# Optimization experiments

Measured on AMD Instinct MI355X. Metric: run time of the kernel, lower is better.

The kernel has to match this reference:

```python
import jax, jax.numpy as jnp
import numpy as np
import math


def _conv(x, w, scale, bias, stride=1):
    # Ultralytics-style Conv: Conv2d(bias=False, pad=k//2) + BatchNorm (folded into
    # per-channel scale/bias) + SiLU
    k = w.shape[-1]
    p = k // 2
    y = jax.lax.conv_general_dilated(x, w, (stride, stride), [(p, p), (p, p)],
                                     dimension_numbers=('NCHW', 'OIHW', 'NCHW'))
    y = y * scale[None, :, None, None] + bias[None, :, None, None]
    return y * jax.nn.sigmoid(y)


def setup_inputs() -> dict:
    key = jax.random.key(0)
    ks = jax.random.split(key, 24)
    B, CH1, CH2, H1, W1, HW = 32, 512, 512, 20, 20, 40
    EMB = 256
    s = 0.05
    half = CH1 // 2
    d = {}
    d['x1'] = jax.random.normal(ks[0], (B, CH1, H1, W1), jnp.float32)
    d['x2'] = jax.random.normal(ks[1], (B, CH2, HW, HW), jnp.float32)
    # CrossAttention params
    d['q_w'] = jax.random.normal(ks[2], (EMB, CH1, 3, 3)) * s
    d['q_s'] = 1.0 + jax.random.normal(ks[3], (EMB,)) * s
    d['q_b'] = jax.random.normal(ks[4], (EMB,)) * s
    d['key_w'] = jax.random.normal(ks[5], (EMB, CH2)) * s
    # MGFAB / CSHA params (CA = channel-MLP sigmoid gate, rate=4)
    d['ca_w1'] = jax.random.normal(ks[6], (half // 4, half)) * s
    d['ca_b1'] = jnp.zeros((half // 4,))
    d['ca_w2'] = jax.random.normal(ks[7], (half, half // 4)) * s
    d['ca_b2'] = jnp.zeros((half,))
    d['sa1_w'] = jax.random.normal(ks[8], (half, half, 3, 3)) * s
    d['sa1_s'] = 1.0 + jax.random.normal(ks[9], (half,)) * s
    d['sa1_b'] = jax.random.normal(ks[10], (half,)) * s
    d['sa2_w'] = jax.random.normal(ks[11], (half, half, 3, 3)) * s
    d['sa2_s'] = 1.0 + jax.random.normal(ks[12], (half,)) * s
    d['sa2_b'] = jax.random.normal(ks[13], (half,)) * s
    d['conv2_w'] = jax.random.normal(ks[14], (CH1, 3 * half, 1, 1)) * s
    d['conv2_s'] = 1.0 + jax.random.normal(ks[15], (CH1,)) * s
    d['conv2_b'] = jax.random.normal(ks[16], (CH1,)) * s
    # conv3 branch (single Conv since patch_size[0] < 5)
    d['c3_w'] = jax.random.normal(ks[17], (CH2, CH2, 3, 3)) * s
    d['c3_s'] = 1.0 + jax.random.normal(ks[18], (CH2,)) * s
    d['c3_b'] = jax.random.normal(ks[19], (CH2,)) * s
    return d


def _forward(x1, x2, q_w, q_s, q_b, key_w, ca_w1, ca_b1, ca_w2, ca_b2,
             sa1_w, sa1_s, sa1_b, sa2_w, sa2_s, sa2_b,
             conv2_w, conv2_s, conv2_b, c3_w, c3_s, c3_b):
    NH, PH, PW = 8, 4, 4
    b, c, h, w = x2.shape
    cH = c // NH                       # channels per head
    nph, npw = h // PH, w // PW        # patch grid
    L = nph * npw                      # number of patches == number of q tokens

    # ---- CrossAttention ----
    # value: per-head flattened patches [b*NH, L, cH*PH*PW] (row-major over h,w)
    v = x2.reshape(b * NH, cH, nph, PH, npw, PW).transpose(0, 2, 4, 1, 3, 5)
    v = v.reshape(b * NH, L, cH * PH * PW)
    # key: avg-pool each patch -> linear(c -> emb) -> split heads
    kp = x2.reshape(b, c, nph, PH, npw, PW).mean(axis=(3, 5))  # [b, c, nph, npw]
    k = jnp.einsum('bcl,ec->ble', kp.reshape(b, c, L), key_w)  # [b, L, EMB]
    dh = k.shape[-1] // NH
    k = k.reshape(b, L, NH, dh).transpose(0, 2, 1, 3).reshape(b * NH, L, dh)
    # query: stride-2 conv on x1 -> tokens -> split heads
    q = _conv(x1, q_w, q_s, q_b, stride=2)                     # [b, EMB, nph, npw]
    q = q.reshape(b, -1, L).transpose(0, 2, 1)                 # [b, L, EMB]
    q = q.reshape(b, L, NH, dh).transpose(0, 2, 1, 3).reshape(b * NH, L, dh)
    score = jnp.einsum('nqd,nkd->nqk', q, k) / math.sqrt(dh)
    wts = jax.nn.softmax(score, axis=-1)                       # dropout = identity (eval)
    y = jnp.einsum('nqk,nkv->nqv', wts, v)                     # [b*NH, L, cH*PH*PW]
    # reassemble patches back into [b, c, h, w]
    attn = y.reshape(b, NH, nph, npw, cH, PH, PW).transpose(0, 1, 4, 2, 5, 3, 6)
    attn = attn.reshape(b, c, h, w)

    # ---- conv3 branch with residual ----
    x2_out = _conv(attn, c3_w, c3_s, c3_b) + attn

    x1_up = jnp.repeat(jnp.repeat(x1, 2, axis=2), 2, axis=3)   # [b, ch1, h, w]
    half = x1_up.shape[1] // 2
    a0, a1 = x1_up[:, :half], x1_up[:, half:]
    # CA: channel MLP gate
    xp = a1.transpose(0, 2, 3, 1)                              # [b, h, w, half]
    att = jnp.maximum(xp @ ca_w1.T + ca_b1, 0.0) @ ca_w2.T + ca_b2
    x_ca = a1 * jax.nn.sigmoid(att.transpose(0, 3, 1, 2))
    # SA: two 3x3 Convs + residual
    x_sa = _conv(_conv(x_ca, sa1_w, sa1_s, sa1_b), sa2_w, sa2_s, sa2_b)
    a2 = x_sa + x_ca
    cat = jnp.concatenate([a0, a1, a2], axis=1)                # [b, 3*half, h, w]
    x1_out = _conv(cat, conv2_w, conv2_s, conv2_b)             # [b, ch1, h, w]

    return jnp.concatenate([x1_out, x2_out], axis=1)           # [b, ch1+ch2, h, w]


def reference(x1, x2, q_w, q_s, q_b, key_w, ca_w1, ca_b1, ca_w2, ca_b2,
              sa1_w, sa1_s, sa1_b, sa2_w, sa2_s, sa2_b,
              conv2_w, conv2_s, conv2_b, c3_w, c3_s, c3_b):
    return _forward(x1, x2, q_w, q_s, q_b, key_w, ca_w1, ca_b1, ca_w2, ca_b2,
                    sa1_w, sa1_s, sa1_b, sa2_w, sa2_s, sa2_b,
                    conv2_w, conv2_s, conv2_b, c3_w, c3_s, c3_b)
```

## Files before the change

kernel.cpp:

```cpp
#include <hip/hip_runtime.h>
#include <hip/hip_bf16.h>

using bf16 = __hip_bfloat16;
using bf16x2 = __hip_bfloat162;
typedef __attribute__((ext_vector_type(8))) short short8;
typedef __attribute__((ext_vector_type(4))) float f32x4;

__device__ __forceinline__ float b2f(bf16 v) { return __bfloat162float(v); }
__device__ __forceinline__ bf16 f2b(float v) { return __float2bfloat16(v); }

__device__ __forceinline__ void gload_lds16(const bf16* g, bf16* l)
{
    __builtin_amdgcn_global_load_lds(
        (const __attribute__((address_space(1))) void*)g,
        (__attribute__((address_space(3))) void*)l,
        16, 0, 0);
}

#define PH_BAR() do { __builtin_amdgcn_sched_barrier(0); __builtin_amdgcn_s_barrier(); __builtin_amdgcn_sched_barrier(0); } while (0)
#define WAIT_LGKM0() do { asm volatile("s_waitcnt lgkmcnt(0)" ::: "memory"); __builtin_amdgcn_sched_barrier(0); } while (0)
#define WAIT_VM0() do { asm volatile("s_waitcnt vmcnt(0)" ::: "memory"); __builtin_amdgcn_sched_barrier(0); } while (0)
#define WAIT_VM2() do { asm volatile("s_waitcnt vmcnt(2)" ::: "memory"); __builtin_amdgcn_sched_barrier(0); } while (0)
#define WAIT_VM4() do { asm volatile("s_waitcnt vmcnt(4)" ::: "memory"); __builtin_amdgcn_sched_barrier(0); } while (0)

__global__ __launch_bounds__(256) void nchw_to_nhwc(const float* __restrict__ in,
                                                    bf16* __restrict__ out,
                                                    int C, int H, int W, int pad)
{
    __shared__ bf16 tile[64][68];
    const int S = H * W;
    const int HP = H + 2 * pad, WP = W + 2 * pad;
    const int b = blockIdx.x, s0 = blockIdx.y * 64, c0 = blockIdx.z * 64;
    const int t = threadIdx.x;
    const int a = t & 63, q = t >> 6;
#pragma unroll
    for (int i = 0; i < 16; ++i) {
        int cl = q + i * 4;
        int s = s0 + a;
        tile[cl][a] = (s < S) ? f2b(in[((size_t)b * C + c0 + cl) * S + s]) : f2b(0.f);
    }
    __syncthreads();
#pragma unroll
    for (int i = 0; i < 16; ++i) {
        int sl = q + i * 4;
        int s = s0 + sl;
        if (s < S) {
            int y = s / W, x = s - (s / W) * W;
            out[(((size_t)b * HP + y + pad) * WP + x + pad) * C + c0 + a] = tile[a][sl];
        }
    }
}

__global__ __launch_bounds__(256) void halo_zero(bf16* __restrict__ buf, int W, int C)
{
    const int b = blockIdx.x, y = blockIdx.y;
    const int P = W + 2;
    const bf16 z = f2b(0.f);
    bf16* row = buf + ((size_t)b * P + y) * P * C;
    if (y == 0 || y == P - 1) {
        for (int i = threadIdx.x; i < P * C; i += 256) row[i] = z;
    } else {
        for (int i = threadIdx.x; i < 2 * C; i += 256) {
            const int x = (i < C) ? 0 : P - 1;
            const int c = (i < C) ? i : i - C;
            row[(size_t)x * C + c] = z;
        }
    }
}

__global__ __launch_bounds__(256) void pack_out(const bf16* __restrict__ x1o,
                                                const bf16* __restrict__ x2o,
                                                float* __restrict__ out)
{
    __shared__ bf16 tile[64][68];
    const int b = blockIdx.x, s0 = blockIdx.y * 64, ch0 = blockIdx.z * 64;
    const bf16* src = (ch0 < 512) ? x1o : x2o;
    const int c0 = ch0 & 511;
    const int t = threadIdx.x;
    const int a = t & 63, q = t >> 6;
#pragma unroll
    for (int i = 0; i < 16; ++i) {
        int sl = q + i * 4;
        tile[sl][a] = src[((size_t)b * 1600 + s0 + sl) * 512 + c0 + a];
    }
    __syncthreads();
#pragma unroll
    for (int i = 0; i < 16; ++i) {
        int cl = q + i * 4;
        out[((size_t)b * 1024 + ch0 + cl) * 1600 + s0 + a] = b2f(tile[a][cl]);
    }
}

__global__ __launch_bounds__(256) void reorder_w(const float* __restrict__ w,
                                                 bf16* __restrict__ wr,
                                                 int C, int total)
{
    int i = blockIdx.x * 256 + threadIdx.x;
    if (i >= total) return;
    int nineC = 9 * C;
    int o = i / nineC;
    int r = i - o * nineC;
    int tap = r / C;
    int c = r - tap * C;
    wr[i] = f2b(w[((size_t)o * C + c) * 9 + tap]);
}

__global__ __launch_bounds__(256) void f32_to_bf16(const float* __restrict__ in,
                                                   bf16* __restrict__ out, int n)
{
    int i = blockIdx.x * 256 + threadIdx.x;
    if (i < n) out[i] = f2b(in[i]);
}

__global__ __launch_bounds__(256) void pool_kp(const bf16* __restrict__ x2n,
                                               bf16* __restrict__ kp)
{
    const int p = blockIdx.x;
    const int b = p / 100, l = p - (p / 100) * 100;
    const int ph = l / 10, pw = l - (l / 10) * 10;
    const int t = threadIdx.x;
    const bf16x2* base = (const bf16x2*)(x2n + (((size_t)(b * 40 + ph * 4) * 40) + pw * 4) * 512) + t;
    float sx = 0.f, sy = 0.f;
#pragma unroll
    for (int py = 0; py < 4; ++py)
#pragma unroll
        for (int px = 0; px < 4; ++px) {
            float2 v = __bfloat1622float2(base[(py * 40 + px) * 256]);
            sx += v.x; sy += v.y;
        }
    ((bf16x2*)(kp + (size_t)p * 512))[t] = __float22bfloat162_rn(make_float2(sx * 0.0625f, sy * 0.0625f));
}

__global__ __launch_bounds__(256) void ca_mlp(const bf16* __restrict__ x1n,
                                              const float* __restrict__ w1, const float* __restrict__ b1,
                                              const float* __restrict__ w2, const float* __restrict__ b2,
                                              bf16* __restrict__ xca)
{
    __shared__ float a1v[256];
    __shared__ float part[4][64];
    __shared__ float hid[64];
    const int blk = blockIdx.x;
    const int b = blk / 400;
    const int rem = blk - b * 400;
    const int y = rem / 20, x = rem - (rem / 20) * 20;
    const int t = threadIdx.x;
    const bf16* src = x1n + ((size_t)(b * 22 + y + 1) * 22 + x + 1) * 512 + 256;
    a1v[t] = b2f(src[t]);
    __syncthreads();
    {
        const int h = t & 63, seg = t >> 6;
        float acc = 0.f;
        const float* wp = w1 + (size_t)h * 256 + seg * 64;
        const float* ap = a1v + seg * 64;
#pragma unroll 8
        for (int c = 0; c < 64; ++c) acc += wp[c] * ap[c];
        part[seg][h] = acc;
    }
    __syncthreads();
    if (t < 64)
        hid[t] = fmaxf(part[0][t] + part[1][t] + part[2][t] + part[3][t] + b1[t], 0.f);
    __syncthreads();
    float acc2 = b2[t];
    const float* w2p = w2 + (size_t)t * 64;
#pragma unroll 8
    for (int h = 0; h < 64; ++h) acc2 += w2p[h] * hid[h];
    const float g = 1.f / (1.f + __expf(-acc2));
    const bf16 o = f2b(a1v[t] * g);
    const size_t obase = ((size_t)(b * 42 + 2 * y + 1) * 42 + 2 * x + 1) * 256 + t;
    xca[obase] = o;
    xca[obase + 256] = o;
    xca[obase + 42 * 256] = o;
    xca[obase + 42 * 256 + 256] = o;
}

__global__ __launch_bounds__(256, 1)
void attn_kernel(const float* __restrict__ q, const float* __restrict__ k,
                 const bf16* __restrict__ x2n, bf16* __restrict__ attn)
{
    __shared__ float sc[100][100];
    __shared__ bf16 wT[100][104];
    const int t = threadIdx.x;
    const int n = blockIdx.x;
    const int b = n >> 3, hd = n & 7;
    const float* qn = q + (size_t)n * 3200;
    const float* kn = k + (size_t)n * 3200;
    for (int e = t; e < 10000; e += 256) {
        const int i = e / 100;
        const int j = e - i * 100;
        const float4* qa = (const float4*)(qn + i * 32);
        const float4* ka = (const float4*)(kn + j * 32);
        float d = 0.f;
#pragma unroll
        for (int u = 0; u < 8; ++u) {
            float4 xv = qa[u], yv = ka[u];
            d += xv.x * yv.x + xv.y * yv.y + xv.z * yv.z + xv.w * yv.w;
        }
        sc[i][j] = d * 0.17677669529663687f;
    }
    __syncthreads();
    if (t < 100) {
        float mx = -1e30f;
        for (int j = 0; j < 100; ++j) mx = fmaxf(mx, sc[t][j]);
        float s = 0.f;
        for (int j = 0; j < 100; ++j) s += __expf(sc[t][j] - mx);
        const float inv = 1.f / s;
        for (int j = 0; j < 100; ++j) wT[j][t] = f2b(__expf(sc[t][j] - mx) * inv);
    }
    __syncthreads();
    const int ch0 = (t & 15) * 4;
    const int pix = t >> 4;
    const int py = pix >> 2, px = pix & 3;
    const bf16* vbase = x2n + (((size_t)(b * 40 + py) * 40) + px) * 512 + hd * 64 + ch0;
    for (int ql0 = 0; ql0 < 100; ql0 += 20) {
        float2 a0[20], a1[20];
#pragma unroll
        for (int i = 0; i < 20; ++i) { a0[i] = make_float2(0.f, 0.f); a1[i] = make_float2(0.f, 0.f); }
        for (int l = 0; l < 100; ++l) {
            const int ph = l / 10, pw = l - (l / 10) * 10;
            const bf16* vp = vbase + ((size_t)(ph * 160 + pw * 4)) * 512;
            const float2 v01 = __bfloat1622float2(*(const bf16x2*)vp);
            const float2 v23 = __bfloat1622float2(*(const bf16x2*)(vp + 2));
            const bf16x2* wp = (const bf16x2*)&wT[l][ql0];
#pragma unroll
            for (int ii = 0; ii < 10; ++ii) {
                const float2 w2 = __bfloat1622float2(wp[ii]);
                a0[ii * 2 + 0].x += w2.x * v01.x; a0[ii * 2 + 0].y += w2.x * v01.y;
                a1[ii * 2 + 0].x += w2.x * v23.x; a1[ii * 2 + 0].y += w2.x * v23.y;
                a0[ii * 2 + 1].x += w2.y * v01.x; a0[ii * 2 + 1].y += w2.y * v01.y;
                a1[ii * 2 + 1].x += w2.y * v23.x; a1[ii * 2 + 1].y += w2.y * v23.y;
            }
        }
#pragma unroll
        for (int i = 0; i < 20; ++i) {
            const int ql = ql0 + i;
            const int ph = ql / 10, pw = ql - (ql / 10) * 10;
            bf16* op = attn + (((size_t)(b * 42 + ph * 4 + py + 1) * 42) + pw * 4 + px + 1) * 512 + hd * 64 + ch0;
            *(bf16x2*)op = __float22bfloat162_rn(a0[i]);
            *(bf16x2*)(op + 2) = __float22bfloat162_rn(a1[i]);
        }
    }
}

enum ConvMode { M_QCONV = 0, M_SA1 = 1, M_SA2 = 2, M_C3 = 3, M_CONV2 = 4, M_KPROJ = 5 };

template <int MODE>
__global__ __launch_bounds__(256, 2)
void conv_mfma(const bf16* __restrict__ in, const bf16* __restrict__ wr,
               const float* __restrict__ scale, const float* __restrict__ bias,
               float* __restrict__ outf)
{
    constexpr int CIN  = 512;
    constexpr int TAPS = (MODE == M_KPROJ) ? 1 : 9;
    constexpr int STR  = 2;
    constexpr int HP   = 22;
    constexpr int WOUT = 10;
    constexpr int K    = TAPS * CIN;
    constexpr int KD   = (TAPS == 9) ? 3 : 1;

    __shared__ bf16 Al[128][64];
    __shared__ bf16 Bl[128][64];

    const int t = threadIdx.x;
    const int p0 = blockIdx.x * 128;
    const int n0 = blockIdx.y * 128;

    int s_row[4], s_dst8[4], s_src8[4], s_b[4], s_oy[4], s_ox[4];
    const bf16* bB[4];
#pragma unroll
    for (int i = 0; i < 4; ++i) {
        const int task = t + i * 256;
        const int row = task >> 3, chk = task & 7;
        s_row[i] = row;
        s_dst8[i] = chk * 8;
        s_src8[i] = (chk ^ (row & 7)) * 8;
        const int p = p0 + row;
        const int bb = p / 100;
        const int s = p - bb * 100;
        s_b[i] = bb;
        s_oy[i] = s / WOUT;
        s_ox[i] = s - s_oy[i] * WOUT;
        bB[i] = wr + (size_t)(n0 + row) * K + s_src8[i];
    }

    const bf16* aP1[4];
    if (MODE == M_KPROJ) {
#pragma unroll
        for (int i = 0; i < 4; ++i)
            aP1[i] = in + (size_t)(p0 + s_row[i]) * 512 + s_src8[i];
    }

    const int lane = t & 63;
    const int wv = t >> 6;
    const int m_off = (wv >> 1) * 64;
    const int n_off = (wv & 1) * 64;
    const int fr = lane & 15;
    const int qd = lane >> 4;
    const int xa = (fr & 7) << 4;

    f32x4 acc[4][4];
#pragma unroll
    for (int mi = 0; mi < 4; ++mi)
#pragma unroll
        for (int ni = 0; ni < 4; ++ni)
            acc[mi][ni] = (f32x4){0.f, 0.f, 0.f, 0.f};

    for (int ky = 0; ky < KD; ++ky)
    for (int kx = 0; kx < KD; ++kx) {
        const bf16* aT[4];
        if (TAPS == 9) {
#pragma unroll
            for (int i = 0; i < 4; ++i)
                aT[i] = in + ((size_t)((s_b[i] * HP + s_oy[i] * STR + ky) * HP) + s_ox[i] * STR + kx) * CIN + s_src8[i];
        }
        const int kk0 = (ky * KD + kx) * CIN;
        for (int c0 = 0; c0 < CIN; c0 += 64) {
#pragma unroll
            for (int i = 0; i < 4; ++i) {
                const bf16* sa = (MODE == M_KPROJ) ? (aP1[i] + c0) : (aT[i] + c0);
                gload_lds16(sa, &Al[s_row[i]][s_dst8[i]]);
            }
#pragma unroll
            for (int i = 0; i < 4; ++i)
                gload_lds16(bB[i] + (kk0 + c0), &Bl[s_row[i]][s_dst8[i]]);
            __syncthreads();
#pragma unroll
            for (int ks = 0; ks < 2; ++ks) {
                short8 af[4], bfr[4];
                const int coff = (ks * 64 + qd * 16) ^ xa;
#pragma unroll
                for (int mi = 0; mi < 4; ++mi)
                    af[mi] = *(const short8*)((const char*)&Al[m_off + mi * 16 + fr][0] + coff);
#pragma unroll
                for (int ni = 0; ni < 4; ++ni)
                    bfr[ni] = *(const short8*)((const char*)&Bl[n_off + ni * 16 + fr][0] + coff);
#pragma unroll
                for (int mi = 0; mi < 4; ++mi)
#pragma unroll
                    for (int ni = 0; ni < 4; ++ni)
                        acc[mi][ni] = __builtin_amdgcn_mfma_f32_16x16x32_bf16(af[mi], bfr[ni], acc[mi][ni], 0, 0, 0);
            }
            __syncthreads();
        }
    }

#pragma unroll
    for (int ni = 0; ni < 4; ++ni) {
        const int nn = n0 + n_off + ni * 16 + fr;
        float scv = 1.f, bsv = 0.f;
        if (MODE != M_KPROJ) { scv = scale[nn]; bsv = bias[nn]; }
#pragma unroll
        for (int mi = 0; mi < 4; ++mi) {
            const int mb = p0 + m_off + mi * 16 + qd * 4;
#pragma unroll
            for (int r = 0; r < 4; ++r) {
                const int p = mb + r;
                const float v = acc[mi][ni][r];
                const int bb = p / 100, l = p - (p / 100) * 100;
                if (MODE == M_KPROJ) {
                    outf[(((size_t)(bb * 8 + (nn >> 5))) * 100 + l) * 32 + (nn & 31)] = v;
                } else {
                    const float y = v * scv + bsv;
                    const float a = y / (1.f + __expf(-y));
                    outf[(((size_t)(bb * 8 + (nn >> 5))) * 100 + l) * 32 + (nn & 31)] = a;
                }
            }
        }
    }
}

template <int MODE>
__device__ __forceinline__ void conv_body256(
    const bf16* __restrict__ in, const bf16* __restrict__ in2,
    const bf16* __restrict__ wr, const float* __restrict__ scale,
    const float* __restrict__ bias, const bf16* __restrict__ resid,
    bf16* __restrict__ outb, bf16* lA, bf16* lB,
    int mtile, int ntile)
{
    constexpr int CIN  = (MODE == M_C3) ? 512 : (MODE == M_CONV2 ? 768 : 256);
    constexpr int TAPS = (MODE == M_CONV2) ? 1 : 9;
    constexpr int K    = TAPS * CIN;
    constexpr int NT   = K / 64;
    constexpr int CPT  = CIN / 64;
    constexpr int L2C  = (CPT == 8) ? 3 : 2;
    constexpr int HP   = 42;

    const int t = threadIdx.x;
    const int p0 = mtile * 256;
    const int n0 = ntile * 256;

    const int row64 = t >> 3;
    const int chk = t & 7;
    const int src8 = (chk ^ (row64 & 7)) * 8;
    const int dst8 = chk * 8;

    const bf16* aBase[4];
    const bf16* aBase2[4];
#pragma unroll
    for (int si = 0; si < 4; ++si) {
        const int p = p0 + si * 64 + row64;
        const int b = p / 1600;
        const int s = p - b * 1600;
        const int oy = s / 40, ox = s - (s / 40) * 40;
        if (MODE == M_CONV2) {
            aBase[si]  = in  + ((size_t)(b * 22 + (oy >> 1) + 1) * 22 + (ox >> 1) + 1) * 512 + src8;
            aBase2[si] = in2 + ((size_t)(b * 1600 + oy * 40 + ox)) * 256 + src8;
        } else {
            aBase[si]  = in  + ((size_t)(b * HP + oy) * HP + ox) * CIN + src8;
            aBase2[si] = nullptr;
        }
    }
    const bf16* bBase[4];
#pragma unroll
    for (int si = 0; si < 4; ++si)
        bBase[si] = wr + (size_t)(n0 + si * 64 + row64) * K + src8;

    const int lane = t & 63;
    const int wv = t >> 6;
    const int m_off = (wv >> 2) * 128;
    const int n_off = (wv & 3) * 64;
    const int fr = lane & 15;
    const int qd = lane >> 4;
    const int xa = (fr & 7) << 4;

    f32x4 acc[8][4];
#pragma unroll
    for (int mi = 0; mi < 8; ++mi)
#pragma unroll
        for (int ni = 0; ni < 4; ++ni)
            acc[mi][ni] = (f32x4){0.f, 0.f, 0.f, 0.f};

#define LDA8(buf, rrow, kkk) \
    (*(const short8*)((const char*)lA + (buf) * 32768 + (rrow) * 128 + ((((kkk) * 64) + qd * 16) ^ xa)))
#define LDB8(buf, rrow, kkk) \
    (*(const short8*)((const char*)lB + (buf) * 32768 + (rrow) * 128 + ((((kkk) * 64) + qd * 16) ^ xa)))

#pragma unroll
    for (int si = 0; si < 4; ++si)
        gload_lds16(aBase[si], lA + (si * 64 + row64) * 64 + dst8);
#pragma unroll
    for (int si = 0; si < 4; ++si)
        gload_lds16(bBase[si], lB + (si * 64 + row64) * 64 + dst8);
    asm volatile("s_waitcnt vmcnt(0)" ::: "memory");
    __syncthreads();

#pragma clang loop unroll(disable)
    for (int kt = 0; kt < NT; ++kt) {
        const int cur = kt & 1;
        const int nxt = cur ^ 1;
        const int ktn = kt + 1;
        const bool pf = (ktn < NT);
        int offAn = 0, c0n = 0;
        if (pf) {
            if (MODE == M_CONV2) {
                c0n = ktn * 64;
            } else {
                const int tap = ktn >> L2C;
                const int ci = ktn & (CPT - 1);
                const int ky = tap / 3, kx = tap - ky * 3;
                offAn = (ky * HP + kx) * CIN + ci * 64;
            }
        }
        const int offBn = ktn * 64;

        auto stA = [&](int si) {
            const bf16* sa;
            if (MODE == M_CONV2) sa = (c0n < 512) ? (aBase[si] + c0n) : (aBase2[si] + (c0n - 512));
            else sa = aBase[si] + offAn;
            gload_lds16(sa, lA + nxt * 16384 + (si * 64 + row64) * 64 + dst8);
        };
        auto stB = [&](int si) {
            gload_lds16(bBase[si] + offBn, lB + nxt * 16384 + (si * 64 + row64) * 64 + dst8);
        };

        short8 af[4][2], bfr[4][2];

#pragma unroll
        for (int m4 = 0; m4 < 4; ++m4) {
            af[m4][0] = LDA8(cur, m_off + m4 * 16 + fr, 0);
            af[m4][1] = LDA8(cur, m_off + m4 * 16 + fr, 1);
        }
#pragma unroll
        for (int n4 = 0; n4 < 4; ++n4) {
            bfr[n4][0] = LDB8(cur, n_off + n4 * 16 + fr, 0);
            bfr[n4][1] = LDB8(cur, n_off + n4 * 16 + fr, 1);
        }
        if (pf) { stA(0); stA(2); stB(0); stB(1); }
        PH_BAR();
        WAIT_LGKM0();
        __builtin_amdgcn_s_setprio(1);
#pragma unroll
        for (int m4 = 0; m4 < 4; ++m4)
#pragma unroll
            for (int n4 = 0; n4 < 4; ++n4) {
                acc[m4][n4] = __builtin_amdgcn_mfma_f32_16x16x32_bf16(af[m4][0], bfr[n4][0], acc[m4][n4], 0, 0, 0);
                acc[m4][n4] = __builtin_amdgcn_mfma_f32_16x16x32_bf16(af[m4][1], bfr[n4][1], acc[m4][n4], 0, 0, 0);
            }
        __builtin_amdgcn_s_setprio(0);
        if (pf) { WAIT_VM4(); } else { WAIT_VM0(); }
        PH_BAR();

#pragma unroll
        for (int m4 = 0; m4 < 4; ++m4) {
            af[m4][0] = LDA8(cur, m_off + (4 + m4) * 16 + fr, 0);
            af[m4][1] = LDA8(cur, m_off + (4 + m4) * 16 + fr, 1);
        }
        if (pf) { stB(2); stB(3); stA(1); stA(3); }
        PH_BAR();
        WAIT_LGKM0();
        __builtin_amdgcn_s_setprio(1);
#pragma unroll
        for (int m4 = 0; m4 < 4; ++m4)
#pragma unroll
            for (int n4 = 0; n4 < 4; ++n4) {
                acc[4 + m4][n4] = __builtin_amdgcn_mfma_f32_16x16x32_bf16(af[m4][0], bfr[n4][0], acc[4 + m4][n4], 0, 0, 0);
                acc[4 + m4][n4] = __builtin_amdgcn_mfma_f32_16x16x32_bf16(af[m4][1], bfr[n4][1], acc[4 + m4][n4], 0, 0, 0);
            }
        __builtin_amdgcn_s_setprio(0);
        if (pf) { WAIT_VM2(); }
        PH_BAR();
    }
#undef LDA8
#undef LDB8

#pragma unroll
    for (int ni = 0; ni < 4; ++ni) {
        const int nn = n0 + n_off + ni * 16 + fr;
        const float scv = scale[nn];
        const float bsv = bias[nn];
#pragma unroll
        for (int mi = 0; mi < 8; ++mi) {
            const int mb = p0 + m_off + mi * 16 + qd * 4;
#pragma unroll
            for (int r = 0; r < 4; ++r) {
                const int p = mb + r;
                const float y = acc[mi][ni][r] * scv + bsv;
                const float a = y / (1.f + __expf(-y));
                if (MODE == M_SA1) {
                    const int bb = p / 1600; const int s = p - bb * 1600;
                    const int oy = s / 40, ox = s - (s / 40) * 40;
                    outb[(((size_t)(bb * 42 + oy + 1)) * 42 + ox + 1) * 256 + nn] = f2b(a);
                } else if (MODE == M_SA2) {
                    const int bb = p / 1600; const int s = p - bb * 1600;
                    const int oy = s / 40, ox = s - (s / 40) * 40;
                    const size_t roff = (((size_t)(bb * 42 + oy + 1)) * 42 + ox + 1) * 256 + nn;
                    outb[(size_t)p * 256 + nn] = f2b(a + b2f(resid[roff]));
                } else if (MODE == M_C3) {
                    const int bb = p / 1600; const int s = p - bb * 1600;
                    const int oy = s / 40, ox = s - (s / 40) * 40;
                    const size_t roff = (((size_t)(bb * 42 + oy + 1)) * 42 + ox + 1) * 512 + nn;
                    outb[(size_t)p * 512 + nn] = f2b(a + b2f(resid[roff]));
                } else {
                    outb[(size_t)p * 512 + nn] = f2b(a);
                }
            }
        }
    }
}

template <int MODE>
__global__ __launch_bounds__(512, 2)
void conv_mfma256(const bf16* __restrict__ in, const bf16* __restrict__ in2,
                  const bf16* __restrict__ wr,
                  const float* __restrict__ scale, const float* __restrict__ bias,
                  const bf16* __restrict__ resid,
                  bf16* __restrict__ outb)
{
    __shared__ bf16 Al[2][256][64];
    __shared__ bf16 Bl[2][256][64];
    int mtile, ntile;
    if (MODE == M_CONV2 || MODE == M_C3) { mtile = blockIdx.x >> 1; ntile = blockIdx.x & 1; }
    else { mtile = blockIdx.x; ntile = 0; }
    conv_body256<MODE>(in, in2, wr, scale, bias, resid, outb,
                       &Al[0][0][0], &Bl[0][0][0], mtile, ntile);
}

__global__ __launch_bounds__(512, 2)
void conv_c3_sa1(const bf16* __restrict__ attn, const bf16* __restrict__ wc3,
                 const float* __restrict__ c3_s, const float* __restrict__ c3_b,
                 bf16* __restrict__ x2o,
                 const bf16* __restrict__ xca, const bf16* __restrict__ wsa1,
                 const float* __restrict__ sa1_s, const float* __restrict__ sa1_b,
                 bf16* __restrict__ tbuf)
{
    __shared__ bf16 Al[2][256][64];
    __shared__ bf16 Bl[2][256][64];
    const int bx = blockIdx.x;
    if (bx < 400) {
        conv_body256<M_C3>(attn, nullptr, wc3, c3_s, c3_b, attn, x2o,
                           &Al[0][0][0], &Bl[0][0][0], bx >> 1, bx & 1);
    } else {
        conv_body256<M_SA1>(xca, nullptr, wsa1, sa1_s, sa1_b, nullptr, tbuf,
                            &Al[0][0][0], &Bl[0][0][0], bx - 400, 0);
    }
}

extern "C" void kernel_launch(void* const* d_in, const int* in_sizes, int n_in,
                              void* d_out, int out_size, void* d_ws, size_t ws_size,
                              hipStream_t stream)
{
    const float* x1      = (const float*)d_in[0];
    const float* x2      = (const float*)d_in[1];
    const float* q_w     = (const float*)d_in[2];
    const float* q_s     = (const float*)d_in[3];
    const float* q_b     = (const float*)d_in[4];
    const float* key_w   = (const float*)d_in[5];
    const float* ca_w1   = (const float*)d_in[6];
    const float* ca_b1   = (const float*)d_in[7];
    const float* ca_w2   = (const float*)d_in[8];
    const float* ca_b2   = (const float*)d_in[9];
    const float* sa1_w   = (const float*)d_in[10];
    const float* sa1_s   = (const float*)d_in[11];
    const float* sa1_b   = (const float*)d_in[12];
    const float* sa2_w   = (const float*)d_in[13];
    const float* sa2_s   = (const float*)d_in[14];
    const float* sa2_b   = (const float*)d_in[15];
    const float* conv2_w = (const float*)d_in[16];
    const float* conv2_s = (const float*)d_in[17];
    const float* conv2_b = (const float*)d_in[18];
    const float* c3_w    = (const float*)d_in[19];
    const float* c3_s    = (const float*)d_in[20];
    const float* c3_b    = (const float*)d_in[21];

    char* ws = (char*)d_ws;
    const size_t o_x1n  = 0;
    const size_t o_x2n  = 15859712;
    const size_t o_attn = 68288512;
    const size_t o_xca  = 126091264;
    const size_t o_tbuf = 154992640;
    const size_t o_a2   = 183894016;
    const size_t o_ws1  = 210108416;
    const size_t o_ws2  = 211288064;
    const size_t o_wc2  = 212467712;
    const size_t o_k    = o_tbuf;
    const size_t o_q    = o_tbuf + 3276800;
    const size_t o_wkey = o_tbuf + 6553600;
    const size_t o_kp   = o_a2;
    const size_t o_wq   = o_a2 + 3276800;
    const size_t o_wc3  = o_a2 + 5636096;

    bf16*  x1n    = (bf16*)(ws + o_x1n);
    bf16*  x2n    = (bf16*)(ws + o_x2n);
    float* k_attn = (float*)(ws + o_k);
    float* q_attn = (float*)(ws + o_q);
    bf16*  attn   = (bf16*)(ws + o_attn);
    bf16*  xca    = (bf16*)(ws + o_xca);
    bf16*  tbuf   = (bf16*)(ws + o_tbuf);
    bf16*  a2     = (bf16*)(ws + o_a2);
    bf16*  wq     = (bf16*)(ws + o_wq);
    bf16*  wc3    = (bf16*)(ws + o_wc3);
    bf16*  wsa1   = (bf16*)(ws + o_ws1);
    bf16*  wsa2   = (bf16*)(ws + o_ws2);
    bf16*  kp     = (bf16*)(ws + o_kp);
    bf16*  wkey   = (bf16*)(ws + o_wkey);
    bf16*  wc2    = (bf16*)(ws + o_wc2);
    bf16*  x2o    = (bf16*)(ws + o_x2n);
    bf16*  x1o    = (bf16*)(ws + o_attn);

    const dim3 blk(256);
    const dim3 blk512(512);

    halo_zero<<<dim3(32, 22), blk, 0, stream>>>(x1n, 20, 512);
    halo_zero<<<dim3(32, 42), blk, 0, stream>>>(xca, 40, 256);
    halo_zero<<<dim3(32, 42), blk, 0, stream>>>(attn, 40, 512);

    nchw_to_nhwc<<<dim3(32, 7, 8), blk, 0, stream>>>(x1, x1n, 512, 20, 20, 1);
    nchw_to_nhwc<<<dim3(32, 25, 8), blk, 0, stream>>>(x2, x2n, 512, 40, 40, 0);
    reorder_w<<<4608, blk, 0, stream>>>(q_w,  wq,   512, 256 * 512 * 9);
    reorder_w<<<9216, blk, 0, stream>>>(c3_w, wc3,  512, 512 * 512 * 9);
    reorder_w<<<2304, blk, 0, stream>>>(sa1_w, wsa1, 256, 256 * 256 * 9);
    reorder_w<<<2304, blk, 0, stream>>>(sa2_w, wsa2, 256, 256 * 256 * 9);
    f32_to_bf16<<<512, blk, 0, stream>>>(key_w, wkey, 256 * 512);
    f32_to_bf16<<<1536, blk, 0, stream>>>(conv2_w, wc2, 512 * 768);
    pool_kp<<<3200, blk, 0, stream>>>(x2n, kp);

    conv_mfma<M_KPROJ><<<dim3(25, 2), blk, 0, stream>>>(kp, wkey, nullptr, nullptr, k_attn);
    conv_mfma<M_QCONV><<<dim3(25, 2), blk, 0, stream>>>(x1n, wq, q_s, q_b, q_attn);

    attn_kernel<<<256, blk, 0, stream>>>(q_attn, k_attn, x2n, attn);

    halo_zero<<<dim3(32, 42), blk, 0, stream>>>(tbuf, 40, 256);

    ca_mlp<<<12800, blk, 0, stream>>>(x1n, ca_w1, ca_b1, ca_w2, ca_b2, xca);

    conv_c3_sa1<<<600, blk512, 0, stream>>>(attn, wc3, c3_s, c3_b, x2o,
                                            xca, wsa1, sa1_s, sa1_b, tbuf);

    conv_mfma256<M_SA2><<<200, blk512, 0, stream>>>(tbuf, nullptr, wsa2,
        sa2_s, sa2_b, xca, a2);
    conv_mfma256<M_CONV2><<<400, blk512, 0, stream>>>(x1n, a2, wc2,
        conv2_s, conv2_b, nullptr, x1o);

    pack_out<<<dim3(32, 25, 16), blk, 0, stream>>>(x1o, x2o, (float*)d_out);

    (void)in_sizes; (void)n_in; (void)out_size; (void)ws_size;
}
```

Before: 1.427 ms.

## Split GEMM main loop into four phases interleaving B loads and prefetches

Splits each K-iteration of the MFMA GEMM main loop from two phases into four. B fragments are read from LDS in two halves, and the global-to-LDS prefetches (stB/stA) are spread across the phases with adjusted vmcnt waits (6 instead of 4). The aim is finer interleaving of LDS reads, async global loads and MFMA work so that memory latency hides better behind compute. In exchange it adds more workgroup barriers per iteration, which may add synchronisation overhead.

```diff
diff --git a/kernel.cpp b/kernel.cpp
--- a/kernel.cpp
+++ b/kernel.cpp
@@ -21,7 +21,7 @@
 #define WAIT_LGKM0() do { asm volatile("s_waitcnt lgkmcnt(0)" ::: "memory"); __builtin_amdgcn_sched_barrier(0); } while (0)
 #define WAIT_VM0() do { asm volatile("s_waitcnt vmcnt(0)" ::: "memory"); __builtin_amdgcn_sched_barrier(0); } while (0)
 #define WAIT_VM2() do { asm volatile("s_waitcnt vmcnt(2)" ::: "memory"); __builtin_amdgcn_sched_barrier(0); } while (0)
-#define WAIT_VM4() do { asm volatile("s_waitcnt vmcnt(4)" ::: "memory"); __builtin_amdgcn_sched_barrier(0); } while (0)
+#define WAIT_VM6() do { asm volatile("s_waitcnt vmcnt(6)" ::: "memory"); __builtin_amdgcn_sched_barrier(0); } while (0)
 
 __global__ __launch_bounds__(256) void nchw_to_nhwc(const float* __restrict__ in,
                                                     bf16* __restrict__ out,
@@ -480,23 +480,42 @@
             af[m4][1] = LDA8(cur, m_off + m4 * 16 + fr, 1);
         }
 #pragma unroll
-        for (int n4 = 0; n4 < 4; ++n4) {
-            bfr[n4][0] = LDB8(cur, n_off + n4 * 16 + fr, 0);
-            bfr[n4][1] = LDB8(cur, n_off + n4 * 16 + fr, 1);
-        }
-        if (pf) { stA(0); stA(2); stB(0); stB(1); }
+        for (int n2 = 0; n2 < 2; ++n2) {
+            bfr[n2][0] = LDB8(cur, n_off + n2 * 16 + fr, 0);
+            bfr[n2][1] = LDB8(cur, n_off + n2 * 16 + fr, 1);
+        }
+        if (pf) { stB(0); stB(1); stB(2); }
         PH_BAR();
         WAIT_LGKM0();
         __builtin_amdgcn_s_setprio(1);
 #pragma unroll
         for (int m4 = 0; m4 < 4; ++m4)
 #pragma unroll
-            for (int n4 = 0; n4 < 4; ++n4) {
-                acc[m4][n4] = __builtin_amdgcn_mfma_f32_16x16x32_bf16(af[m4][0], bfr[n4][0], acc[m4][n4], 0, 0, 0);
-                acc[m4][n4] = __builtin_amdgcn_mfma_f32_16x16x32_bf16(af[m4][1], bfr[n4][1], acc[m4][n4], 0, 0, 0);
+            for (int n2 = 0; n2 < 2; ++n2) {
+                acc[m4][n2] = __builtin_amdgcn_mfma_f32_16x16x32_bf16(af[m4][0], bfr[n2][0], acc[m4][n2], 0, 0, 0);
+                acc[m4][n2] = __builtin_amdgcn_mfma_f32_16x16x32_bf16(af[m4][1], bfr[n2][1], acc[m4][n2], 0, 0, 0);
             }
         __builtin_amdgcn_s_setprio(0);
-        if (pf) { WAIT_VM4(); } else { WAIT_VM0(); }
+        PH_BAR();
+
+#pragma unroll
+        for (int n2 = 2; n2 < 4; ++n2) {
+            bfr[n2][0] = LDB8(cur, n_off + n2 * 16 + fr, 0);
+            bfr[n2][1] = LDB8(cur, n_off + n2 * 16 + fr, 1);
+        }
+        if (pf) { stB(3); stA(0); stA(2); }
+        PH_BAR();
+        WAIT_LGKM0();
+        __builtin_amdgcn_s_setprio(1);
+#pragma unroll
+        for (int m4 = 0; m4 < 4; ++m4)
+#pragma unroll
+            for (int n2 = 2; n2 < 4; ++n2) {
+                acc[m4][n2] = __builtin_amdgcn_mfma_f32_16x16x32_bf16(af[m4][0], bfr[n2][0], acc[m4][n2], 0, 0, 0);
+                acc[m4][n2] = __builtin_amdgcn_mfma_f32_16x16x32_bf16(af[m4][1], bfr[n2][1], acc[m4][n2], 0, 0, 0);
+            }
+        __builtin_amdgcn_s_setprio(0);
+        if (pf) { WAIT_VM6(); } else { WAIT_VM0(); }
         PH_BAR();
 
 #pragma unroll
@@ -504,16 +523,27 @@
             af[m4][0] = LDA8(cur, m_off + (4 + m4) * 16 + fr, 0);
             af[m4][1] = LDA8(cur, m_off + (4 + m4) * 16 + fr, 1);
         }
-        if (pf) { stB(2); stB(3); stA(1); stA(3); }
         PH_BAR();
         WAIT_LGKM0();
         __builtin_amdgcn_s_setprio(1);
 #pragma unroll
         for (int m4 = 0; m4 < 4; ++m4)
 #pragma unroll
-            for (int n4 = 0; n4 < 4; ++n4) {
-                acc[4 + m4][n4] = __builtin_amdgcn_mfma_f32_16x16x32_bf16(af[m4][0], bfr[n4][0], acc[4 + m4][n4], 0, 0, 0);
-                acc[4 + m4][n4] = __builtin_amdgcn_mfma_f32_16x16x32_bf16(af[m4][1], bfr[n4][1], acc[4 + m4][n4], 0, 0, 0);
+            for (int n2 = 0; n2 < 2; ++n2) {
+                acc[4 + m4][n2] = __builtin_amdgcn_mfma_f32_16x16x32_bf16(af[m4][0], bfr[n2][0], acc[4 + m4][n2], 0, 0, 0);
+                acc[4 + m4][n2] = __builtin_amdgcn_mfma_f32_16x16x32_bf16(af[m4][1], bfr[n2][1], acc[4 + m4][n2], 0, 0, 0);
+            }
+        __builtin_amdgcn_s_setprio(0);
+        PH_BAR();
+
+        if (pf) { stA(1); stA(3); }
+        __builtin_amdgcn_s_setprio(1);
+#pragma unroll
+        for (int m4 = 0; m4 < 4; ++m4)
+#pragma unroll
+            for (int n2 = 2; n2 < 4; ++n2) {
+                acc[4 + m4][n2] = __builtin_amdgcn_mfma_f32_16x16x32_bf16(af[m4][0], bfr[n2][0], acc[4 + m4][n2], 0, 0, 0);
+                acc[4 + m4][n2] = __builtin_amdgcn_mfma_f32_16x16x32_bf16(af[m4][1], bfr[n2][1], acc[4 + m4][n2], 0, 0, 0);
             }
         __builtin_amdgcn_s_setprio(0);
         if (pf) { WAIT_VM2(); }
```

New measurement: 1.422 ms. No clear change (-0.3%).
